# Kernel optimization log

Measured on AMD Instinct MI355X. Metric: run time of the kernel, lower is better.

The kernel has to match this reference:

```python
import jax, jax.numpy as jnp
import numpy as np

B, T, C, H = 2, 2048, 1024, 16
D = C // H  # head dim = 64
EPS = 1e-5


def setup_inputs() -> dict:
    key = jax.random.key(0)
    k1, k2, k3 = jax.random.split(key, 3)
    x = jax.random.normal(k1, (B, T, C), dtype=jnp.float32)
    W_attn = jax.random.normal(k2, (3 * C, C), dtype=jnp.float32) * 0.02
    W_proj = jax.random.normal(k3, (C, C), dtype=jnp.float32) * 0.02
    # standard RoPE inverse frequencies, one per rotation pair (D//2)
    rope_freqs = 1.0 / (10000.0 ** (jnp.arange(D // 2, dtype=jnp.float32) * 2.0 / D))
    ln_weight = jnp.ones((C,), dtype=jnp.float32)
    ln_bias = jnp.zeros((C,), dtype=jnp.float32)
    return {"x": x, "rope_freqs": rope_freqs, "W_attn": W_attn,
            "W_proj": W_proj, "ln_weight": ln_weight, "ln_bias": ln_bias}


def _apply_rope(q, k, freqs):
    # q,k: [B,H,S,D]; matches torch apply_rope: split even/odd, concat halves
    S = q.shape[-2]
    theta = jnp.arange(S, dtype=q.dtype)[:, None] * freqs[None, :]  # [S, D/2]
    sin_t, cos_t = jnp.sin(theta), jnp.cos(theta)

    def rot(t):
        t1, t2 = t[..., 0::2], t[..., 1::2]
        return jnp.concatenate([t1 * cos_t - t2 * sin_t,
                                t1 * sin_t + t2 * cos_t], axis=-1)

    return rot(q), rot(k)


def reference(x, rope_freqs, W_attn, W_proj, ln_weight, ln_bias):
    Bv, Tv, Cv = x.shape
    qkv = x @ W_attn.T                      # [B,T,3C] (F.linear, no bias)
    q, k, v = jnp.split(qkv, 3, axis=-1)
    resh = lambda t: t.reshape(Bv, Tv, H, D).transpose(0, 2, 1, 3)  # [B,H,T,D]
    q, k, v = resh(q), resh(k), resh(v)
    q, k = _apply_rope(q, k, rope_freqs)
    scale = 1.0 / jnp.sqrt(jnp.asarray(D, dtype=x.dtype))
    scores = jnp.einsum('bhqd,bhkd->bhqk', q, k) * scale
    causal = jnp.tril(jnp.ones((Tv, Tv), dtype=bool))
    scores = jnp.where(causal[None, None], scores, -jnp.inf)
    att = jax.nn.softmax(scores, axis=-1)
    y = jnp.einsum('bhqk,bhkd->bhqd', att, v)
    y = y.transpose(0, 2, 1, 3).reshape(Bv, Tv, Cv)
    y = y @ W_proj.T                        # c_proj (bias=False)
    # resid dropout is identity in eval; LayerNorm (eps=1e-5, biased var)
    mean = jnp.mean(y, axis=-1, keepdims=True)
    var = jnp.mean(jnp.square(y - mean), axis=-1, keepdims=True)
    return (y - mean) / jnp.sqrt(var + EPS) * ln_weight + ln_bias
```

## Files before the change

kernel.cpp:

```cpp
#include <hip/hip_runtime.h>
#include <hip/hip_bf16.h>
#include <math.h>

typedef short bf16x8 __attribute__((ext_vector_type(8)));
typedef float f32x4 __attribute__((ext_vector_type(4)));

#define T_SEQ 2048
#define C_DIM 1024
#define H_HEADS 16
#define D_HEAD 64
#define BT 4096
#define C3 3072
#define BH 32

static __device__ inline unsigned short bf_bits(float f) {
    __hip_bfloat16 h = __float2bfloat16(f);
    unsigned short u;
    __builtin_memcpy(&u, &h, 2);
    return u;
}

static __device__ inline unsigned int cvtpk(float lo, float hi) {
    unsigned int r;
    asm("v_cvt_pk_bf16_f32 %0, %1, %2" : "=v"(r) : "v"(lo), "v"(hi));
    return r;
}

__device__ __forceinline__ void gload16(const void* g, void* l) {
    __builtin_amdgcn_global_load_lds(
        (const __attribute__((address_space(1))) void*)g,
        (__attribute__((address_space(3))) void*)l, 16, 0, 0);
}

__device__ __forceinline__ int swz(int r) {
    return ((((r & 3) ^ ((r >> 3) & 3)) | (((r >> 3) & 1) << 2)) << 3);
}

__global__ void cast_f32_bf16(const float* __restrict__ in,
                              __hip_bfloat16* __restrict__ out, int n4) {
    int i = blockIdx.x * blockDim.x + threadIdx.x;
    if (i >= n4) return;
    float4 v = reinterpret_cast<const float4*>(in)[i];
    ushort4 o;
    o.x = bf_bits(v.x); o.y = bf_bits(v.y); o.z = bf_bits(v.z); o.w = bf_bits(v.w);
    reinterpret_cast<ushort4*>(out)[i] = o;
}

template<int OUT_BF16, int BN>
__global__ __launch_bounds__(256) void gemm_bt(
    const __hip_bfloat16* __restrict__ A,
    const __hip_bfloat16* __restrict__ Bw,
    void* __restrict__ Cout, int M, int N, int K) {
    __shared__ __hip_bfloat16 As[128][64];
    __shared__ __hip_bfloat16 Bs[BN][64];
    const int t = threadIdx.x;
    const int lane = t & 63, w = t >> 6;
    const int wr = w >> 1, wc = w & 1;
    const int l15 = lane & 15, lg = lane >> 4;
    const int m0 = blockIdx.y * 128, n0 = blockIdx.x * BN;

    const int srow = lane >> 3;
    const int scol = ((lane & 7) ^ srow) * 8;
    const int xr = (l15 & 7) << 3;

    constexpr int NF = BN / 32;
    f32x4 acc[4][NF];
    f32x4 zero4 = {0.f, 0.f, 0.f, 0.f};
#pragma unroll
    for (int m = 0; m < 4; m++)
#pragma unroll
        for (int n = 0; n < NF; n++) acc[m][n] = zero4;

    const int nt = K >> 6;
    for (int tk = 0; tk < nt; tk++) {
        const int k0 = tk << 6;
#pragma unroll
        for (int i = 0; i < 4; i++) {
            int rbase = w * 32 + i * 8;
            gload16(&A[(size_t)(m0 + rbase + srow) * K + k0 + scol], &As[rbase][0]);
        }
#pragma unroll
        for (int i = 0; i < NF; i++) {
            int rbase = w * (BN / 4) + i * 8;
            gload16(&Bw[(size_t)(n0 + rbase + srow) * K + k0 + scol], &Bs[rbase][0]);
        }
        __syncthreads();
#pragma unroll
        for (int kk = 0; kk < 2; kk++) {
            bf16x8 a[4], b[NF];
            const int co = (kk * 32 + lg * 8) ^ xr;
#pragma unroll
            for (int m = 0; m < 4; m++)
                a[m] = *reinterpret_cast<const bf16x8*>(&As[wr * 64 + m * 16 + l15][co]);
#pragma unroll
            for (int n = 0; n < NF; n++)
                b[n] = *reinterpret_cast<const bf16x8*>(&Bs[wc * (BN / 2) + n * 16 + l15][co]);
            __builtin_amdgcn_s_setprio(1);
#pragma unroll
            for (int m = 0; m < 4; m++)
#pragma unroll
                for (int n = 0; n < NF; n++)
                    acc[m][n] = __builtin_amdgcn_mfma_f32_16x16x32_bf16(a[m], b[n], acc[m][n], 0, 0, 0);
            __builtin_amdgcn_s_setprio(0);
        }
        __syncthreads();
    }

#pragma unroll
    for (int m = 0; m < 4; m++)
#pragma unroll
        for (int n = 0; n < NF; n++)
#pragma unroll
            for (int jj = 0; jj < 4; jj++) {
                int row = m0 + wr * 64 + m * 16 + lg * 4 + jj;
                int col = n0 + wc * (BN / 2) + n * 16 + l15;
                float v = acc[m][n][jj];
                if (OUT_BF16)
                    ((__hip_bfloat16*)Cout)[(size_t)row * N + col] = __float2bfloat16(v);
                else
                    ((float*)Cout)[(size_t)row * N + col] = v;
            }
}

__global__ void rope_qk(const __hip_bfloat16* __restrict__ qkv,
                        const float* __restrict__ freqs,
                        __hip_bfloat16* __restrict__ q_s,
                        __hip_bfloat16* __restrict__ k_s) {
    int idx = blockIdx.x * 256 + threadIdx.x;
    int i = idx & 31;
    int h = (idx >> 5) & 15;
    int bt = idx >> 9;
    int b = bt >> 11;
    int tp = bt & 2047;
    float th = (float)tp * freqs[i];
    float sn = sinf(th), cs = cosf(th);
    size_t qoff = (size_t)bt * C3 + h * 64;
    float q1 = __bfloat162float(qkv[qoff + 2 * i]);
    float q2 = __bfloat162float(qkv[qoff + 2 * i + 1]);
    float k1 = __bfloat162float(qkv[qoff + C_DIM + 2 * i]);
    float k2 = __bfloat162float(qkv[qoff + C_DIM + 2 * i + 1]);
    size_t obase = ((size_t)(b * H_HEADS + h) * T_SEQ + tp) * D_HEAD;
    const float sc = 0.125f * 1.44269504f;
    q_s[obase + i]      = __float2bfloat16((q1 * cs - q2 * sn) * sc);
    q_s[obase + 32 + i] = __float2bfloat16((q1 * sn + q2 * cs) * sc);
    k_s[obase + i]      = __float2bfloat16(k1 * cs - k2 * sn);
    k_s[obase + 32 + i] = __float2bfloat16(k1 * sn + k2 * cs);
}

__global__ __launch_bounds__(256) void transpose_v(const __hip_bfloat16* __restrict__ qkv,
                                                   __hip_bfloat16* __restrict__ v_t) {
    __shared__ __hip_bfloat16 tile[64][72];
    const int bh = blockIdx.y, tt = blockIdx.x;
    const int b = bh >> 4, h = bh & 15;
    const int t = threadIdx.x;
    const int r = t >> 2, c0 = (t & 3) * 16;
    const __hip_bfloat16* src = qkv + (size_t)(b * T_SEQ + tt * 64 + r) * C3 + 2 * C_DIM + h * 64 + c0;
    uint4 v0 = reinterpret_cast<const uint4*>(src)[0];
    uint4 v1 = reinterpret_cast<const uint4*>(src)[1];
    *reinterpret_cast<uint4*>(&tile[r][c0]) = v0;
    *reinterpret_cast<uint4*>(&tile[r][c0 + 8]) = v1;
    __syncthreads();
    const int d = t >> 2;
    ushort out[16];
#pragma unroll
    for (int i = 0; i < 16; i++) {
        __hip_bfloat16 x = tile[c0 + i][d];
        __builtin_memcpy(&out[i], &x, 2);
    }
    __hip_bfloat16* dst = v_t + (size_t)bh * D_HEAD * T_SEQ + (size_t)d * T_SEQ + tt * 64 + c0;
    reinterpret_cast<uint4*>(dst)[0] = *reinterpret_cast<uint4*>(&out[0]);
    reinterpret_cast<uint4*>(dst)[1] = *reinterpret_cast<uint4*>(&out[8]);
}

__global__ __launch_bounds__(256, 4) void attn_kernel(
    const __hip_bfloat16* __restrict__ q_s,
    const __hip_bfloat16* __restrict__ k_s,
    const __hip_bfloat16* __restrict__ v_t,
    __hip_bfloat16* __restrict__ y) {
    __shared__ ushort Kbuf[2][64 * 64];
    __shared__ ushort Vbuf[2][64 * 64];

    const int bid = blockIdx.x;
    const int qt = 31 - (bid >> 5);
    const int bh = bid & 31;
    const int t = threadIdx.x, lane = t & 63, w = t >> 6;
    const int l15 = lane & 15, lg = lane >> 4;
    const size_t hbase = (size_t)bh * T_SEQ * D_HEAD;
    const int qr = qt * 64 + w * 16 + l15;

    bf16x8 aq[2];
#pragma unroll
    for (int dd = 0; dd < 2; dd++)
        aq[dd] = *reinterpret_cast<const bf16x8*>(&q_s[hbase + (size_t)qr * 64 + dd * 32 + lg * 8]);

    bf16x8 ones;
#pragma unroll
    for (int i = 0; i < 8; i++) ones[i] = (short)0x3F80;

    f32x4 zero4 = {0.f, 0.f, 0.f, 0.f};
    f32x4 o[4];
#pragma unroll
    for (int dc = 0; dc < 4; dc++) o[dc] = zero4;
    f32x4 lacc = zero4;
    float mr = -INFINITY;

    int koff[4][2], voff[4][2];
#pragma unroll
    for (int c = 0; c < 4; c++) {
        int kro = ((c >> 1) << 5) + ((c & 1) << 2) + ((l15 >> 2) << 3) + (l15 & 3);
        int sz = swz(kro);
#pragma unroll
        for (int dd = 0; dd < 2; dd++)
            koff[c][dd] = kro * 64 + ((dd * 32 + lg * 8) ^ sz);
    }
#pragma unroll
    for (int dc = 0; dc < 4; dc++) {
        int vro = dc * 16 + l15;
        int sz = swz(vro);
#pragma unroll
        for (int dd = 0; dd < 2; dd++)
            voff[dc][dd] = vro * 64 + ((dd * 32 + lg * 8) ^ sz);
    }

    const int srow = t >> 3;
    const int sgr = t & 7;

    auto stageKV = [&](int buf, int kbase) {
#pragma unroll
        for (int i = 0; i < 2; i++) {
            int r = i * 32 + srow;
            int gsw = (sgr ^ (swz(r) >> 3)) * 8;
            gload16(&k_s[hbase + (size_t)(kbase + r) * 64 + gsw],
                    &Kbuf[buf][(i * 32 + w * 8) * 64]);
            gload16(&v_t[hbase + (size_t)r * T_SEQ + kbase + gsw],
                    &Vbuf[buf][(i * 32 + w * 8) * 64]);
        }
    };

    int cur = 0;
    stageKV(0, 0);
    __syncthreads();

    for (int kt = 0; kt <= qt; kt++) {
        const int kt64 = kt << 6;
        if (kt < qt) stageKV(cur ^ 1, kt64 + 64);

        const ushort* Kc = Kbuf[cur];
        const ushort* Vc = Vbuf[cur];
        bf16x8 kf[4][2], av[4][2];
#pragma unroll
        for (int c = 0; c < 4; c++)
#pragma unroll
            for (int dd = 0; dd < 2; dd++)
                kf[c][dd] = *reinterpret_cast<const bf16x8*>(&Kc[koff[c][dd]]);
#pragma unroll
        for (int dc = 0; dc < 4; dc++)
#pragma unroll
            for (int dd = 0; dd < 2; dd++)
                av[dc][dd] = *reinterpret_cast<const bf16x8*>(&Vc[voff[dc][dd]]);

        f32x4 st[4];
        __builtin_amdgcn_s_setprio(1);
#pragma unroll
        for (int c = 0; c < 4; c++) {
            st[c] = zero4;
#pragma unroll
            for (int dd = 0; dd < 2; dd++)
                st[c] = __builtin_amdgcn_mfma_f32_16x16x32_bf16(kf[c][dd], aq[dd], st[c], 0, 0, 0);
        }
        __builtin_amdgcn_s_setprio(0);

        if (kt == qt) {
#pragma unroll
            for (int c = 0; c < 4; c++) {
                int kb = kt64 + ((c >> 1) << 5) + ((c & 1) << 2) + lg * 8;
#pragma unroll
                for (int jj = 0; jj < 4; jj++)
                    if (kb + jj > qr) st[c][jj] = -INFINITY;
            }
        }

        float m0a = fmaxf(st[0][0], st[0][1]), m0b = fmaxf(st[0][2], st[0][3]);
        float m1a = fmaxf(st[1][0], st[1][1]), m1b = fmaxf(st[1][2], st[1][3]);
        float m2a = fmaxf(st[2][0], st[2][1]), m2b = fmaxf(st[2][2], st[2][3]);
        float m3a = fmaxf(st[3][0], st[3][1]), m3b = fmaxf(st[3][2], st[3][3]);
        float lmx = fmaxf(fmaxf(fmaxf(m0a, m0b), fmaxf(m1a, m1b)),
                          fmaxf(fmaxf(m2a, m2b), fmaxf(m3a, m3b)));

        if (__any(lmx - mr > 8.f)) {
            float mx = fmaxf(lmx, __shfl_xor(lmx, 16));
            mx = fmaxf(mx, __shfl_xor(mx, 32));
            float mnew = fmaxf(mr, mx);
            float scl = __builtin_amdgcn_exp2f(mr - mnew);
            mr = mnew;
            lacc[0] *= scl;
#pragma unroll
            for (int dc = 0; dc < 4; dc++)
#pragma unroll
                for (int jj = 0; jj < 4; jj++) o[dc][jj] *= scl;
        }

#pragma unroll
        for (int c = 0; c < 4; c++)
#pragma unroll
            for (int jj = 0; jj < 4; jj++)
                st[c][jj] = __builtin_amdgcn_exp2f(st[c][jj] - mr);

        union { bf16x8 v; unsigned int u[4]; } pf0, pf1;
        pf0.u[0] = cvtpk(st[0][0], st[0][1]);
        pf0.u[1] = cvtpk(st[0][2], st[0][3]);
        pf0.u[2] = cvtpk(st[1][0], st[1][1]);
        pf0.u[3] = cvtpk(st[1][2], st[1][3]);
        pf1.u[0] = cvtpk(st[2][0], st[2][1]);
        pf1.u[1] = cvtpk(st[2][2], st[2][3]);
        pf1.u[2] = cvtpk(st[3][0], st[3][1]);
        pf1.u[3] = cvtpk(st[3][2], st[3][3]);

        __builtin_amdgcn_s_setprio(1);
        lacc = __builtin_amdgcn_mfma_f32_16x16x32_bf16(ones, pf0.v, lacc, 0, 0, 0);
        lacc = __builtin_amdgcn_mfma_f32_16x16x32_bf16(ones, pf1.v, lacc, 0, 0, 0);
#pragma unroll
        for (int dc = 0; dc < 4; dc++) {
            o[dc] = __builtin_amdgcn_mfma_f32_16x16x32_bf16(av[dc][0], pf0.v, o[dc], 0, 0, 0);
            o[dc] = __builtin_amdgcn_mfma_f32_16x16x32_bf16(av[dc][1], pf1.v, o[dc], 0, 0, 0);
        }
        __builtin_amdgcn_s_setprio(0);

        __syncthreads();
        cur ^= 1;
    }

    const int b = bh >> 4, h = bh & 15;
    float inv = 1.f / lacc[0];
#pragma unroll
    for (int dc = 0; dc < 4; dc++) {
        ushort4 ov;
        ov.x = bf_bits(o[dc][0] * inv);
        ov.y = bf_bits(o[dc][1] * inv);
        ov.z = bf_bits(o[dc][2] * inv);
        ov.w = bf_bits(o[dc][3] * inv);
        *reinterpret_cast<ushort4*>(
            &y[(size_t)(b * T_SEQ + qr) * C_DIM + h * 64 + dc * 16 + lg * 4]) = ov;
    }
}

__global__ __launch_bounds__(256) void ln_kernel(const __hip_bfloat16* __restrict__ y2,
                                                 const float* __restrict__ wgt,
                                                 const float* __restrict__ bias,
                                                 float* __restrict__ out) {
    const int row = blockIdx.x;
    const int t = threadIdx.x;
    ushort4 u = reinterpret_cast<const ushort4*>(y2 + (size_t)row * C_DIM)[t];
    float4 v;
    v.x = __bfloat162float(*(__hip_bfloat16*)&u.x);
    v.y = __bfloat162float(*(__hip_bfloat16*)&u.y);
    v.z = __bfloat162float(*(__hip_bfloat16*)&u.z);
    v.w = __bfloat162float(*(__hip_bfloat16*)&u.w);
    float s = v.x + v.y + v.z + v.w;
    float s2 = v.x * v.x + v.y * v.y + v.z * v.z + v.w * v.w;
#pragma unroll
    for (int d = 1; d < 64; d <<= 1) {
        s += __shfl_xor(s, d);
        s2 += __shfl_xor(s2, d);
    }
    __shared__ float ps[4], ps2[4];
    const int lane = t & 63, w = t >> 6;
    if (lane == 0) { ps[w] = s; ps2[w] = s2; }
    __syncthreads();
    s = ps[0] + ps[1] + ps[2] + ps[3];
    s2 = ps2[0] + ps2[1] + ps2[2] + ps2[3];
    float mean = s * (1.f / C_DIM);
    float var = s2 * (1.f / C_DIM) - mean * mean;
    float inv = rsqrtf(var + 1e-5f);
    float4 wv = reinterpret_cast<const float4*>(wgt)[t];
    float4 bv = reinterpret_cast<const float4*>(bias)[t];
    float4 ov;
    ov.x = (v.x - mean) * inv * wv.x + bv.x;
    ov.y = (v.y - mean) * inv * wv.y + bv.y;
    ov.z = (v.z - mean) * inv * wv.z + bv.z;
    ov.w = (v.w - mean) * inv * wv.w + bv.w;
    reinterpret_cast<float4*>(out + (size_t)row * C_DIM)[t] = ov;
}

extern "C" void kernel_launch(void* const* d_in, const int* in_sizes, int n_in,
                              void* d_out, int out_size, void* d_ws, size_t ws_size,
                              hipStream_t stream) {
    const float* x      = (const float*)d_in[0];
    const float* freqs  = (const float*)d_in[1];
    const float* W_attn = (const float*)d_in[2];
    const float* W_proj = (const float*)d_in[3];
    const float* lnw    = (const float*)d_in[4];
    const float* lnb    = (const float*)d_in[5];
    float* out = (float*)d_out;
    char* ws = (char*)d_ws;

    __hip_bfloat16* xb   = (__hip_bfloat16*)(ws);
    __hip_bfloat16* Wab  = (__hip_bfloat16*)(ws + 8388608);
    __hip_bfloat16* Wpb  = (__hip_bfloat16*)(ws + 14680064);
    __hip_bfloat16* qkvb = (__hip_bfloat16*)(ws + 16777216);
    __hip_bfloat16* q_s  = (__hip_bfloat16*)(ws + 41943040);
    __hip_bfloat16* k_s  = (__hip_bfloat16*)(ws + 50331648);
    __hip_bfloat16* v_t  = (__hip_bfloat16*)(ws + 58720256);
    __hip_bfloat16* y_at = (__hip_bfloat16*)(ws + 67108864);
    __hip_bfloat16* y2b  = (__hip_bfloat16*)(ws + 75497472);

    cast_f32_bf16<<<(BT * C_DIM / 4) / 256, 256, 0, stream>>>(x, xb, BT * C_DIM / 4);
    cast_f32_bf16<<<(C3 * C_DIM / 4) / 256, 256, 0, stream>>>(W_attn, Wab, C3 * C_DIM / 4);
    cast_f32_bf16<<<(C_DIM * C_DIM / 4) / 256, 256, 0, stream>>>(W_proj, Wpb, C_DIM * C_DIM / 4);

    gemm_bt<1, 128><<<dim3(C3 / 128, BT / 128), 256, 0, stream>>>(xb, Wab, qkvb, BT, C3, C_DIM);

    rope_qk<<<(BT * H_HEADS * 32) / 256, 256, 0, stream>>>(qkvb, freqs, q_s, k_s);
    transpose_v<<<dim3(T_SEQ / 64, BH), 256, 0, stream>>>(qkvb, v_t);

    attn_kernel<<<1024, 256, 0, stream>>>(q_s, k_s, v_t, y_at);

    gemm_bt<1, 64><<<dim3(C_DIM / 64, BT / 128), 256, 0, stream>>>(y_at, Wpb, y2b, BT, C_DIM, C_DIM);

    ln_kernel<<<BT, 256, 0, stream>>>(y2b, lnw, lnb, out);
}
```

Baseline: 114.5 us.

## Fuse RoPE and V transpose into QKV GEMM epilogue with precomputed sin/cos table

The QKV GEMM gains an epilogue mode that applies RoPE, using a lane shuffle to fetch the paired element, and writes Q/K directly in head-major layout. The same epilogue writes V already transposed. A small kernel precomputes a cos/sin table per position and frequency. This removes the intermediate qkv buffer round trip and two separate kernel launches. In exchange the epilogue does scattered 2-byte stores and table reads, which may be poorly coalesced.

```diff
diff --git a/kernel.cpp b/kernel.cpp
--- a/kernel.cpp
+++ b/kernel.cpp
@@ -46,11 +46,22 @@
     reinterpret_cast<ushort4*>(out)[i] = o;
 }
 
-template<int OUT_BF16, int BN>
+__global__ void rope_table(const float* __restrict__ freqs, float2* __restrict__ tab) {
+    int idx = blockIdx.x * 256 + threadIdx.x;
+    int i = idx & 31, tp = idx >> 5;
+    float th = (float)tp * freqs[i];
+    tab[idx] = make_float2(cosf(th), sinf(th));
+}
+
+template<int MODE, int BN>
 __global__ __launch_bounds__(256) void gemm_bt(
     const __hip_bfloat16* __restrict__ A,
     const __hip_bfloat16* __restrict__ Bw,
-    void* __restrict__ Cout, int M, int N, int K) {
+    void* __restrict__ Cout, int M, int N, int K,
+    const float2* __restrict__ tab,
+    __hip_bfloat16* __restrict__ q_s,
+    __hip_bfloat16* __restrict__ k_s,
+    __hip_bfloat16* __restrict__ v_t) {
     __shared__ __hip_bfloat16 As[128][64];
     __shared__ __hip_bfloat16 Bs[BN][64];
     const int t = threadIdx.x;
@@ -106,6 +117,45 @@
         __syncthreads();
     }
 
+    if (MODE == 2) {
+        const int region = n0 >> 10;
+#pragma unroll
+        for (int m = 0; m < 4; m++)
+#pragma unroll
+            for (int n = 0; n < NF; n++) {
+                const int col = n0 + wc * (BN / 2) + n * 16 + l15;
+                const int d = col & 63;
+                const int h = (col >> 6) & 15;
+                const int row0 = m0 + wr * 64 + m * 16 + lg * 4;
+                const int b = row0 >> 11;
+                const int tp0 = row0 & 2047;
+                if (region < 2) {
+                    const int i = d >> 1, odd = d & 1;
+                    const int dp = (d >> 1) + (odd ? 32 : 0);
+                    __hip_bfloat16* dst = (region == 0) ? q_s : k_s;
+                    const float sc = (region == 0) ? 0.125f * 1.44269504f : 1.0f;
+#pragma unroll
+                    for (int jj = 0; jj < 4; jj++) {
+                        float own = acc[m][n][jj];
+                        float par = __shfl_xor(own, 1);
+                        float2 cs = tab[(tp0 + jj) * 32 + i];
+                        float val = own * cs.x + (odd ? par : -par) * cs.y;
+                        dst[((size_t)(b * H_HEADS + h) * T_SEQ + tp0 + jj) * D_HEAD + dp] =
+                            __float2bfloat16(val * sc);
+                    }
+                } else {
+                    ushort4 ov;
+                    ov.x = bf_bits(acc[m][n][0]);
+                    ov.y = bf_bits(acc[m][n][1]);
+                    ov.z = bf_bits(acc[m][n][2]);
+                    ov.w = bf_bits(acc[m][n][3]);
+                    *reinterpret_cast<ushort4*>(
+                        &v_t[((size_t)(b * H_HEADS + h) * D_HEAD + d) * T_SEQ + tp0]) = ov;
+                }
+            }
+        return;
+    }
+
 #pragma unroll
     for (int m = 0; m < 4; m++)
 #pragma unroll
@@ -115,61 +165,11 @@
                 int row = m0 + wr * 64 + m * 16 + lg * 4 + jj;
                 int col = n0 + wc * (BN / 2) + n * 16 + l15;
                 float v = acc[m][n][jj];
-                if (OUT_BF16)
+                if (MODE == 1)
                     ((__hip_bfloat16*)Cout)[(size_t)row * N + col] = __float2bfloat16(v);
                 else
                     ((float*)Cout)[(size_t)row * N + col] = v;
             }
-}
-
-__global__ void rope_qk(const __hip_bfloat16* __restrict__ qkv,
-                        const float* __restrict__ freqs,
-                        __hip_bfloat16* __restrict__ q_s,
-                        __hip_bfloat16* __restrict__ k_s) {
-    int idx = blockIdx.x * 256 + threadIdx.x;
-    int i = idx & 31;
-    int h = (idx >> 5) & 15;
-    int bt = idx >> 9;
-    int b = bt >> 11;
-    int tp = bt & 2047;
-    float th = (float)tp * freqs[i];
-    float sn = sinf(th), cs = cosf(th);
-    size_t qoff = (size_t)bt * C3 + h * 64;
-    float q1 = __bfloat162float(qkv[qoff + 2 * i]);
-    float q2 = __bfloat162float(qkv[qoff + 2 * i + 1]);
-    float k1 = __bfloat162float(qkv[qoff + C_DIM + 2 * i]);
-    float k2 = __bfloat162float(qkv[qoff + C_DIM + 2 * i + 1]);
-    size_t obase = ((size_t)(b * H_HEADS + h) * T_SEQ + tp) * D_HEAD;
-    const float sc = 0.125f * 1.44269504f;
-    q_s[obase + i]      = __float2bfloat16((q1 * cs - q2 * sn) * sc);
-    q_s[obase + 32 + i] = __float2bfloat16((q1 * sn + q2 * cs) * sc);
-    k_s[obase + i]      = __float2bfloat16(k1 * cs - k2 * sn);
-    k_s[obase + 32 + i] = __float2bfloat16(k1 * sn + k2 * cs);
-}
-
-__global__ __launch_bounds__(256) void transpose_v(const __hip_bfloat16* __restrict__ qkv,
-                                                   __hip_bfloat16* __restrict__ v_t) {
-    __shared__ __hip_bfloat16 tile[64][72];
-    const int bh = blockIdx.y, tt = blockIdx.x;
-    const int b = bh >> 4, h = bh & 15;
-    const int t = threadIdx.x;
-    const int r = t >> 2, c0 = (t & 3) * 16;
-    const __hip_bfloat16* src = qkv + (size_t)(b * T_SEQ + tt * 64 + r) * C3 + 2 * C_DIM + h * 64 + c0;
-    uint4 v0 = reinterpret_cast<const uint4*>(src)[0];
-    uint4 v1 = reinterpret_cast<const uint4*>(src)[1];
-    *reinterpret_cast<uint4*>(&tile[r][c0]) = v0;
-    *reinterpret_cast<uint4*>(&tile[r][c0 + 8]) = v1;
-    __syncthreads();
-    const int d = t >> 2;
-    ushort out[16];
-#pragma unroll
-    for (int i = 0; i < 16; i++) {
-        __hip_bfloat16 x = tile[c0 + i][d];
-        __builtin_memcpy(&out[i], &x, 2);
-    }
-    __hip_bfloat16* dst = v_t + (size_t)bh * D_HEAD * T_SEQ + (size_t)d * T_SEQ + tt * 64 + c0;
-    reinterpret_cast<uint4*>(dst)[0] = *reinterpret_cast<uint4*>(&out[0]);
-    reinterpret_cast<uint4*>(dst)[1] = *reinterpret_cast<uint4*>(&out[8]);
 }
 
 __global__ __launch_bounds__(256, 4) void attn_kernel(
@@ -397,25 +397,25 @@
     __hip_bfloat16* xb   = (__hip_bfloat16*)(ws);
     __hip_bfloat16* Wab  = (__hip_bfloat16*)(ws + 8388608);
     __hip_bfloat16* Wpb  = (__hip_bfloat16*)(ws + 14680064);
-    __hip_bfloat16* qkvb = (__hip_bfloat16*)(ws + 16777216);
+    float2*         tab  = (float2*)(ws + 16777216);
     __hip_bfloat16* q_s  = (__hip_bfloat16*)(ws + 41943040);
     __hip_bfloat16* k_s  = (__hip_bfloat16*)(ws + 50331648);
     __hip_bfloat16* v_t  = (__hip_bfloat16*)(ws + 58720256);
     __hip_bfloat16* y_at = (__hip_bfloat16*)(ws + 67108864);
     __hip_bfloat16* y2b  = (__hip_bfloat16*)(ws + 75497472);
 
+    rope_table<<<(T_SEQ * 32) / 256, 256, 0, stream>>>(freqs, tab);
     cast_f32_bf16<<<(BT * C_DIM / 4) / 256, 256, 0, stream>>>(x, xb, BT * C_DIM / 4);
     cast_f32_bf16<<<(C3 * C_DIM / 4) / 256, 256, 0, stream>>>(W_attn, Wab, C3 * C_DIM / 4);
     cast_f32_bf16<<<(C_DIM * C_DIM / 4) / 256, 256, 0, stream>>>(W_proj, Wpb, C_DIM * C_DIM / 4);
 
-    gemm_bt<1, 128><<<dim3(C3 / 128, BT / 128), 256, 0, stream>>>(xb, Wab, qkvb, BT, C3, C_DIM);
-
-    rope_qk<<<(BT * H_HEADS * 32) / 256, 256, 0, stream>>>(qkvb, freqs, q_s, k_s);
-    transpose_v<<<dim3(T_SEQ / 64, BH), 256, 0, stream>>>(qkvb, v_t);
+    gemm_bt<2, 128><<<dim3(C3 / 128, BT / 128), 256, 0, stream>>>(
+        xb, Wab, nullptr, BT, C3, C_DIM, tab, q_s, k_s, v_t);
 
     attn_kernel<<<1024, 256, 0, stream>>>(q_s, k_s, v_t, y_at);
 
-    gemm_bt<1, 64><<<dim3(C_DIM / 64, BT / 128), 256, 0, stream>>>(y_at, Wpb, y2b, BT, C_DIM, C_DIM);
+    gemm_bt<1, 64><<<dim3(C_DIM / 64, BT / 128), 256, 0, stream>>>(
+        y_at, Wpb, y2b, BT, C_DIM, C_DIM, nullptr, nullptr, nullptr, nullptr);
 
     ln_kernel<<<BT, 256, 0, stream>>>(y2b, lnw, lnb, out);
 }
```

Result: no change. 112.5 us (-1.8%).
